# Performance work log

Hardware: AMD Instinct MI355X
Metric: run time of the kernel (lower is better)

## Reference

```python
import jax, jax.numpy as jnp
import numpy as np

B, T, N, F, O = 4, 8192, 64, 16, 32  # batch, timesteps, vertices, in_feat, out_feat


def setup_inputs() -> dict:
    key = jax.random.key(0)
    ks = jax.random.split(key, 8)
    return {
        "x": jax.random.normal(ks[0], (B, T, N * F), dtype=jnp.float32),
        "adj": jax.random.uniform(ks[1], (N, N), dtype=jnp.float32),
        "W1": jax.random.normal(ks[2], (T,), dtype=jnp.float32) / np.sqrt(T).astype(np.float32),
        "W2": jax.random.normal(ks[3], (F, T), dtype=jnp.float32) / np.sqrt(F).astype(np.float32),
        "W3": jax.random.normal(ks[4], (F,), dtype=jnp.float32) / np.sqrt(F).astype(np.float32),
        "bs": jax.random.normal(ks[5], (1, N, N), dtype=jnp.float32) * 0.02,
        "Vs": jax.random.normal(ks[6], (N, N), dtype=jnp.float32) * 0.02,
        "conv_w": jax.random.normal(ks[7], (O, N * F, 3), dtype=jnp.float32) * 0.02,
    }


def reference(x, adj, W1, W2, W3, bs, Vs, conv_w):
    bz, t, _ = x.shape
    x4 = x.reshape(bz, t, N, F)
    xp = jnp.transpose(x4, (0, 2, 3, 1))  # (B, N, F, T)

    # Spatial attention: S in (B, N, N)
    lhs = jnp.einsum('bnft,t->bnf', xp, W1) @ W2          # (B, N, T)
    rhs = jnp.einsum('f,bnft->bnt', W3, xp)               # (B, N, T)
    product = jnp.einsum('bnt,bmt->bnm', lhs, rhs)        # (B, N, N)
    S = jnp.einsum('nm,bmk->bnk', Vs, jax.nn.sigmoid(product + bs))
    S = jax.nn.softmax(S, axis=1)

    # Apply attention over the vertex dim
    xr = jnp.transpose(x4, (0, 1, 3, 2)).reshape(bz, t * F, N)  # (B, T*F, N)
    xm = jnp.einsum('bpn,bnm->bpm', xr, S)                      # (B, T*F, N)
    xf = jnp.transpose(xm.reshape(bz, t, F, N), (0, 2, 1, 3))   # (B, F, T, N)

    # einsum 'bftn,nn->bftn' == scale by diagonal of adj
    xf = xf * jnp.diagonal(adj)                                 # broadcast over N

    xo = jnp.transpose(xf, (0, 2, 3, 1)).reshape(bz, t, N * F)  # (B, T, N*F)

    # Conv1d(kernel=3, padding=1, no bias), channels-last
    out = jax.lax.conv_general_dilated(
        xo, conv_w,
        window_strides=(1,), padding=((1, 1),),
        dimension_numbers=('NWC', 'OIW', 'NWC'))
    return out  # (B, T, O)
```

## Files before the change

### kernel.cpp

```cpp
#include <hip/hip_runtime.h>
#include <hip/hip_bf16.h>

#define B_ 4
#define T_ 8192
#define N_ 64
#define F_ 16
#define O_ 32

typedef _Float16 half8_t __attribute__((ext_vector_type(8)));
typedef _Float16 half4_t __attribute__((ext_vector_type(4)));
typedef float float4_t __attribute__((ext_vector_type(4)));

#define WS_A1G  0
#define WS_SSC  32768
#define WS_WFT  98304
#define WS_P    524288
#define WS_XH   9437184
#define XH_BYTES ((size_t)B_ * (T_ + 2) * 1024 * sizeof(_Float16))

#define TB_ 32

__global__ __launch_bounds__(256) void kA2(const float* __restrict__ x,
                                           const float* __restrict__ W1,
                                           const float* __restrict__ W2,
                                           const float* __restrict__ W3,
                                           float* __restrict__ P,
                                           _Float16* __restrict__ xh) {
    __shared__ float w2s[16][TB_ + 1];
    __shared__ float w1s[TB_];
    const int b    = blockIdx.x >> 8;
    const int tile = blockIdx.x & 255;
    const int t0   = tile * TB_;
    const int tid  = threadIdx.x;
    const int fq   = tid & 3;

    for (int i = tid; i < 16 * TB_; i += 256) {
        const int f = i >> 5, r = i & 31;
        w2s[f][r] = W2[f * T_ + t0 + r];
    }
    if (tid < TB_) w1s[tid] = W1[t0 + tid];
    __syncthreads();

    float w3v[4];
#pragma unroll
    for (int j = 0; j < 4; ++j) w3v[j] = W3[fq * 4 + j];

    const float* xbase = x + ((size_t)b * T_ + t0) * 1024 + tid * 4;
    _Float16* xrow = xh ? (xh + ((size_t)b * (T_ + 2) + (t0 + 1)) * 1024 + tid * 4)
                        : (_Float16*)nullptr;
    float4_t accA = {0.f, 0.f, 0.f, 0.f};
    float4_t accG = {0.f, 0.f, 0.f, 0.f};

#pragma unroll 8
    for (int r = 0; r < TB_; ++r) {
        float4_t xv = *(const float4_t*)(xbase + (size_t)r * 1024);
        if (xh) {
            half4_t hv;
            hv[0] = (_Float16)xv[0]; hv[1] = (_Float16)xv[1];
            hv[2] = (_Float16)xv[2]; hv[3] = (_Float16)xv[3];
            *(half4_t*)(xrow + (size_t)r * 1024) = hv;
        }
        float v = xv[0] * w3v[0] + xv[1] * w3v[1] + xv[2] * w3v[2] + xv[3] * w3v[3];
        v += __shfl_xor(v, 1);
        v += __shfl_xor(v, 2);
        const float w1r = w1s[r];
#pragma unroll
        for (int j = 0; j < 4; ++j) {
            accA[j] += w1r * xv[j];
            accG[j] += w2s[fq * 4 + j][r] * v;
        }
    }

    if (xh) {
        half4_t z = {(_Float16)0.f, (_Float16)0.f, (_Float16)0.f, (_Float16)0.f};
        if (tile == 0)
            *(half4_t*)(xh + (size_t)b * (T_ + 2) * 1024 + tid * 4) = z;
        if (tile == 255)
            *(half4_t*)(xh + ((size_t)b * (T_ + 2) + T_ + 1) * 1024 + tid * 4) = z;
    }

    float* pb = P + (size_t)blockIdx.x * 2048 + tid * 4;
    *(float4_t*)pb          = accA;
    *(float4_t*)(pb + 1024) = accG;
}

__global__ __launch_bounds__(256) void kR(const float* __restrict__ P,
                                          float* __restrict__ A1G) {
    const int b   = blockIdx.x >> 3;
    const int seg = blockIdx.x & 7;
    const int tid = threadIdx.x;
    const int o4  = tid & 63;
    const int g   = tid >> 6;

    const float* base = P + (size_t)b * 256 * 2048 + seg * 256 + o4 * 4;
    float4_t s = {0.f, 0.f, 0.f, 0.f};
#pragma unroll 4
    for (int tt = 0; tt < 64; ++tt) {
        float4_t v = *(const float4_t*)(base + (size_t)(g * 64 + tt) * 2048);
        s += v;
    }

    __shared__ float4_t red[4][64];
    red[g][o4] = s;
    __syncthreads();
    if (tid < 64) {
        float4_t t = red[0][tid] + red[1][tid] + red[2][tid] + red[3][tid];
        *(float4_t*)(A1G + (size_t)b * 2048 + seg * 256 + tid * 4) = t;
    }
}

__global__ __launch_bounds__(256) void kC(const float* __restrict__ A1G,
                                          const float* __restrict__ bs,
                                          const float* __restrict__ Vs,
                                          const float* __restrict__ adj,
                                          float* __restrict__ Ssc) {
    const int b = blockIdx.x;
    __shared__ float a1[64][17], g[64][17];
    __shared__ float sig[64][64];
    __shared__ float vs[64][64];
    __shared__ float redmx[4][64];
    __shared__ float redsm[4][64];
    const int tid = threadIdx.x;

    for (int i = tid; i < 1024; i += 256) {
        a1[i >> 4][i & 15] = A1G[b * 2048 + i];
        g [i >> 4][i & 15] = A1G[b * 2048 + 1024 + i];
    }
    for (int i = tid; i < 4096; i += 256) vs[i >> 6][i & 63] = Vs[i];
    __syncthreads();

#pragma unroll
    for (int i = 0; i < 16; ++i) {
        const int e = tid + 256 * i, r = e >> 6, c = e & 63;
        float p = 0.f;
#pragma unroll
        for (int f = 0; f < 16; ++f) p += a1[r][f] * g[c][f];
        p += bs[e];
        sig[r][c] = 1.f / (1.f + __expf(-p));
    }
    __syncthreads();

    const int gw = tid >> 6;
    const int c  = tid & 63;
    const int r0 = gw * 16;

    float sc_[64];
#pragma unroll
    for (int m = 0; m < 64; ++m) sc_[m] = sig[m][c];

    float acc[16];
#pragma unroll
    for (int rl = 0; rl < 16; ++rl) {
        const float4_t* vr = (const float4_t*)&vs[r0 + rl][0];
        float sA = 0.f, sB = 0.f, sC = 0.f, sD = 0.f;
#pragma unroll
        for (int m4 = 0; m4 < 4; ++m4) {
            float4_t v0 = vr[m4];
            float4_t v1 = vr[m4 + 4];
            float4_t v2 = vr[m4 + 8];
            float4_t v3 = vr[m4 + 12];
#pragma unroll
            for (int j = 0; j < 4; ++j) {
                sA += v0[j] * sc_[m4 * 4 + j];
                sB += v1[j] * sc_[16 + m4 * 4 + j];
                sC += v2[j] * sc_[32 + m4 * 4 + j];
                sD += v3[j] * sc_[48 + m4 * 4 + j];
            }
        }
        acc[rl] = (sA + sB) + (sC + sD);
    }

    float pmax = -1e30f;
#pragma unroll
    for (int rl = 0; rl < 16; ++rl) pmax = fmaxf(pmax, acc[rl]);
    redmx[gw][c] = pmax;
    __syncthreads();
    const float mx = fmaxf(fmaxf(redmx[0][c], redmx[1][c]),
                           fmaxf(redmx[2][c], redmx[3][c]));

    float psum = 0.f;
#pragma unroll
    for (int rl = 0; rl < 16; ++rl) {
        acc[rl] = __expf(acc[rl] - mx);
        psum += acc[rl];
    }
    redsm[gw][c] = psum;
    __syncthreads();
    const float sum = (redsm[0][c] + redsm[1][c]) + (redsm[2][c] + redsm[3][c]);
    const float scl = adj[c * 64 + c] / sum;

#pragma unroll
    for (int rl = 0; rl < 16; ++rl)
        Ssc[b * 4096 + (r0 + rl) * 64 + c] = acc[rl] * scl;
}

__global__ __launch_bounds__(256) void kD(const float* __restrict__ Ssc,
                                          const float* __restrict__ conv_w,
                                          _Float16* __restrict__ Wft) {
    const int b = blockIdx.x >> 5, o = blockIdx.x & 31;
    __shared__ float ssc[4096];
    __shared__ float cw[3072];
    const int tid = threadIdx.x;
    for (int i = tid; i < 4096; i += 256) ssc[i] = Ssc[b * 4096 + i];
    for (int i = tid; i < 3072; i += 256) cw[i] = conv_w[o * 3072 + i];
    __syncthreads();

#pragma unroll
    for (int i = 0; i < 12; ++i) {
        const int e = tid + 256 * i;
        const int k = e >> 10, rem = e & 1023, m = rem >> 4, f = rem & 15;
        float s = 0.f;
#pragma unroll
        for (int n = 0; n < 64; ++n) s += cw[(n * 16 + f) * 3 + k] * ssc[m * 64 + n];
        Wft[(size_t)(b * 32 + o) * 3072 + e] = (_Float16)s;
    }
}

__global__ __launch_bounds__(256) void kE16(const _Float16* __restrict__ xh,
                                            const _Float16* __restrict__ Wft,
                                            float* __restrict__ out) {
    const int b    = blockIdx.x >> 7;
    const int tile = blockIdx.x & 127;
    const int wave = threadIdx.x >> 6;
    const int lane = threadIdx.x & 63;
    const int q = lane >> 4, l = lane & 15;
    const int t0 = tile * 64 + wave * 16;

    const _Float16* wb0 = Wft + (size_t)(b * 32 + l) * 3072;
    const _Float16* wb1 = wb0 + 16 * 3072;
    const _Float16* xb = xh + ((size_t)b * (T_ + 2) + (t0 + l)) * 1024 + q * 8;

    float4_t acc0 = {0.f, 0.f, 0.f, 0.f};
    float4_t acc1 = {0.f, 0.f, 0.f, 0.f};

#pragma unroll 8
    for (int kk = 0; kk < 96; ++kk) {
        const int K  = kk * 32;
        const int kc = K >> 10;
        const int c0 = K & 1023;

        half8_t af  = *(const half8_t*)(xb + (size_t)kc * 1024 + c0);
        half8_t bf0 = *(const half8_t*)(wb0 + K + q * 8);
        half8_t bf1 = *(const half8_t*)(wb1 + K + q * 8);

        acc0 = __builtin_amdgcn_mfma_f32_16x16x32_f16(af, bf0, acc0, 0, 0, 0);
        acc1 = __builtin_amdgcn_mfma_f32_16x16x32_f16(af, bf1, acc1, 0, 0, 0);
    }

#pragma unroll
    for (int rg = 0; rg < 4; ++rg) {
        const int t = t0 + q * 4 + rg;
        float* op = out + ((size_t)b * T_ + t) * 32;
        op[l]      = acc0[rg];
        op[16 + l] = acc1[rg];
    }
}

__global__ __launch_bounds__(256) void kE32(const float* __restrict__ x,
                                            const _Float16* __restrict__ Wft,
                                            float* __restrict__ out) {
    const int b    = blockIdx.x >> 7;
    const int tile = blockIdx.x & 127;
    const int wave = threadIdx.x >> 6;
    const int lane = threadIdx.x & 63;
    const int q = lane >> 4, l = lane & 15;
    const int t0 = tile * 64 + wave * 16;

    const _Float16* wb0 = Wft + (size_t)(b * 32 + l) * 3072;
    const _Float16* wb1 = wb0 + 16 * 3072;
    const float* xb = x + (size_t)b * T_ * 1024;

    float4_t acc0 = {0.f, 0.f, 0.f, 0.f};
    float4_t acc1 = {0.f, 0.f, 0.f, 0.f};

#pragma unroll 4
    for (int kk = 0; kk < 96; ++kk) {
        const int K  = kk * 32;
        const int kc = K >> 10;
        const int c0 = (K & 1023) + q * 8;
        const int row = t0 + l + kc - 1;
        const bool valid = (unsigned)row < (unsigned)T_;
        const int rc = valid ? row : 0;
        const float sc = valid ? 1.f : 0.f;

        const float* ap = xb + (size_t)rc * 1024 + c0;
        float4_t a0 = *(const float4_t*)ap;
        float4_t a1 = *(const float4_t*)(ap + 4);

        half8_t af;
        af[0] = (_Float16)(a0[0] * sc); af[1] = (_Float16)(a0[1] * sc);
        af[2] = (_Float16)(a0[2] * sc); af[3] = (_Float16)(a0[3] * sc);
        af[4] = (_Float16)(a1[0] * sc); af[5] = (_Float16)(a1[1] * sc);
        af[6] = (_Float16)(a1[2] * sc); af[7] = (_Float16)(a1[3] * sc);

        half8_t bf0 = *(const half8_t*)(wb0 + K + q * 8);
        half8_t bf1 = *(const half8_t*)(wb1 + K + q * 8);

        acc0 = __builtin_amdgcn_mfma_f32_16x16x32_f16(af, bf0, acc0, 0, 0, 0);
        acc1 = __builtin_amdgcn_mfma_f32_16x16x32_f16(af, bf1, acc1, 0, 0, 0);
    }

#pragma unroll
    for (int rg = 0; rg < 4; ++rg) {
        const int t = t0 + q * 4 + rg;
        float* op = out + ((size_t)b * T_ + t) * 32;
        op[l]      = acc0[rg];
        op[16 + l] = acc1[rg];
    }
}

extern "C" void kernel_launch(void* const* d_in, const int* in_sizes, int n_in,
                              void* d_out, int out_size, void* d_ws, size_t ws_size,
                              hipStream_t stream) {
    const float* x      = (const float*)d_in[0];
    const float* adj    = (const float*)d_in[1];
    const float* W1     = (const float*)d_in[2];
    const float* W2     = (const float*)d_in[3];
    const float* W3     = (const float*)d_in[4];
    const float* bs     = (const float*)d_in[5];
    const float* Vs     = (const float*)d_in[6];
    const float* conv_w = (const float*)d_in[7];
    float* out = (float*)d_out;

    char* ws = (char*)d_ws;
    float*    A1G = (float*)(ws + WS_A1G);
    float*    Ssc = (float*)(ws + WS_SSC);
    _Float16* Wft = (_Float16*)(ws + WS_WFT);
    float*    P   = (float*)(ws + WS_P);

    const bool use16 = ws_size >= (size_t)WS_XH + XH_BYTES;
    _Float16* xh = use16 ? (_Float16*)(ws + WS_XH) : (_Float16*)nullptr;

    kA2<<<B_ * (T_ / TB_), 256, 0, stream>>>(x, W1, W2, W3, P, xh);
    kR <<<B_ * 8,          256, 0, stream>>>(P, A1G);
    kC <<<B_,              256, 0, stream>>>(A1G, bs, Vs, adj, Ssc);
    kD <<<B_ * O_,         256, 0, stream>>>(Ssc, conv_w, Wft);
    if (use16) kE16<<<B_ * (T_ / 64), 256, 0, stream>>>(xh, Wft, out);
    else       kE32<<<B_ * (T_ / 64), 256, 0, stream>>>(x, Wft, out);
}
```

Before: 319.1 us.

## Halve time tiles, remap kA2 threads per vertex, split kE16 waves by output half

kA2 now handles 16 timesteps per block instead of 32, which doubles its grid. Each thread processes a full 16-feature vertex row across 4 timesteps, so the shuffle reduction is gone, and partial sums are combined across waves in shared memory before being written out. kR is adjusted for the doubled partial count. kE16 gives each wave one 16-output half for 16 timesteps, which doubles its grid and halves per-wave work. The change aims to raise parallelism and occupancy in the bandwidth-bound passes. In exchange, A-fragment loads in kE16 are duplicated across the two output halves, kA2 uses more registers, and P grows, which needs a larger workspace.

```diff
diff --git a/kernel.cpp b/kernel.cpp
--- a/kernel.cpp
+++ b/kernel.cpp
@@ -15,84 +15,127 @@
 #define WS_SSC  32768
 #define WS_WFT  98304
 #define WS_P    524288
-#define WS_XH   9437184
+#define WS_XH   17825792
 #define XH_BYTES ((size_t)B_ * (T_ + 2) * 1024 * sizeof(_Float16))
 
-#define TB_ 32
-
-__global__ __launch_bounds__(256) void kA2(const float* __restrict__ x,
-                                           const float* __restrict__ W1,
-                                           const float* __restrict__ W2,
-                                           const float* __restrict__ W3,
-                                           float* __restrict__ P,
-                                           _Float16* __restrict__ xh) {
+#define TB_ 16
+
+__global__ __launch_bounds__(256, 6) void kA2(const float* __restrict__ x,
+                                              const float* __restrict__ W1,
+                                              const float* __restrict__ W2,
+                                              const float* __restrict__ W3,
+                                              float* __restrict__ P,
+                                              _Float16* __restrict__ xh) {
     __shared__ float w2s[16][TB_ + 1];
     __shared__ float w1s[TB_];
-    const int b    = blockIdx.x >> 8;
-    const int tile = blockIdx.x & 255;
+    __shared__ float red[4][64][16];
+    const int b    = blockIdx.x >> 9;
+    const int tile = blockIdx.x & 511;
     const int t0   = tile * TB_;
     const int tid  = threadIdx.x;
-    const int fq   = tid & 3;
-
-    for (int i = tid; i < 16 * TB_; i += 256) {
-        const int f = i >> 5, r = i & 31;
+    const int w    = tid >> 6;
+    const int n    = tid & 63;
+
+    {
+        const int f = tid >> 4, r = tid & 15;
         w2s[f][r] = W2[f * T_ + t0 + r];
-    }
-    if (tid < TB_) w1s[tid] = W1[t0 + tid];
-    __syncthreads();
-
-    float w3v[4];
-#pragma unroll
-    for (int j = 0; j < 4; ++j) w3v[j] = W3[fq * 4 + j];
-
-    const float* xbase = x + ((size_t)b * T_ + t0) * 1024 + tid * 4;
-    _Float16* xrow = xh ? (xh + ((size_t)b * (T_ + 2) + (t0 + 1)) * 1024 + tid * 4)
-                        : (_Float16*)nullptr;
-    float4_t accA = {0.f, 0.f, 0.f, 0.f};
-    float4_t accG = {0.f, 0.f, 0.f, 0.f};
-
-#pragma unroll 8
-    for (int r = 0; r < TB_; ++r) {
-        float4_t xv = *(const float4_t*)(xbase + (size_t)r * 1024);
+        if (tid < TB_) w1s[tid] = W1[t0 + tid];
+    }
+    __syncthreads();
+
+    float w3v[16];
+#pragma unroll
+    for (int f = 0; f < 16; ++f) w3v[f] = W3[f];
+
+    float accA[16], accG[16];
+#pragma unroll
+    for (int f = 0; f < 16; ++f) { accA[f] = 0.f; accG[f] = 0.f; }
+
+    const float* xrow0 = x + ((size_t)b * T_ + t0 + w * 4) * 1024 + n * 16;
+    _Float16* xh0 = xh ? (xh + ((size_t)b * (T_ + 2) + t0 + 1 + w * 4) * 1024 + n * 16)
+                       : (_Float16*)nullptr;
+
+#pragma unroll
+    for (int i = 0; i < 4; ++i) {
+        const int r = w * 4 + i;
+        const float* xp = xrow0 + (size_t)i * 1024;
+        float4_t x0 = *(const float4_t*)(xp);
+        float4_t x1 = *(const float4_t*)(xp + 4);
+        float4_t x2 = *(const float4_t*)(xp + 8);
+        float4_t x3 = *(const float4_t*)(xp + 12);
+
         if (xh) {
-            half4_t hv;
-            hv[0] = (_Float16)xv[0]; hv[1] = (_Float16)xv[1];
-            hv[2] = (_Float16)xv[2]; hv[3] = (_Float16)xv[3];
-            *(half4_t*)(xrow + (size_t)r * 1024) = hv;
+            half8_t h0, h1;
+#pragma unroll
+            for (int j = 0; j < 4; ++j) {
+                h0[j]     = (_Float16)x0[j]; h0[4 + j] = (_Float16)x1[j];
+                h1[j]     = (_Float16)x2[j]; h1[4 + j] = (_Float16)x3[j];
+            }
+            _Float16* hp = xh0 + (size_t)i * 1024;
+            *(half8_t*)(hp)     = h0;
+            *(half8_t*)(hp + 8) = h1;
         }
-        float v = xv[0] * w3v[0] + xv[1] * w3v[1] + xv[2] * w3v[2] + xv[3] * w3v[3];
-        v += __shfl_xor(v, 1);
-        v += __shfl_xor(v, 2);
+
+        float v = 0.f;
+#pragma unroll
+        for (int j = 0; j < 4; ++j) {
+            v += x0[j] * w3v[j]      + x1[j] * w3v[4 + j]
+               + x2[j] * w3v[8 + j]  + x3[j] * w3v[12 + j];
+        }
         const float w1r = w1s[r];
 #pragma unroll
         for (int j = 0; j < 4; ++j) {
-            accA[j] += w1r * xv[j];
-            accG[j] += w2s[fq * 4 + j][r] * v;
+            accA[j]      += w1r * x0[j];  accA[4 + j]  += w1r * x1[j];
+            accA[8 + j]  += w1r * x2[j];  accA[12 + j] += w1r * x3[j];
         }
+#pragma unroll
+        for (int f = 0; f < 16; ++f) accG[f] += w2s[f][r] * v;
     }
 
     if (xh) {
         half4_t z = {(_Float16)0.f, (_Float16)0.f, (_Float16)0.f, (_Float16)0.f};
         if (tile == 0)
             *(half4_t*)(xh + (size_t)b * (T_ + 2) * 1024 + tid * 4) = z;
-        if (tile == 255)
+        if (tile == 511)
             *(half4_t*)(xh + ((size_t)b * (T_ + 2) + T_ + 1) * 1024 + tid * 4) = z;
     }
 
-    float* pb = P + (size_t)blockIdx.x * 2048 + tid * 4;
-    *(float4_t*)pb          = accA;
-    *(float4_t*)(pb + 1024) = accG;
+#pragma unroll
+    for (int f = 0; f < 16; ++f) red[w][n][f] = accA[f];
+    __syncthreads();
+    {
+        const int nn = tid >> 2, fb = (tid & 3) * 4;
+        float4_t s;
+#pragma unroll
+        for (int j = 0; j < 4; ++j)
+            s[j] = red[0][nn][fb + j] + red[1][nn][fb + j]
+                 + red[2][nn][fb + j] + red[3][nn][fb + j];
+        *(float4_t*)(P + (size_t)blockIdx.x * 2048 + nn * 16 + fb) = s;
+    }
+    __syncthreads();
+#pragma unroll
+    for (int f = 0; f < 16; ++f) red[w][n][f] = accG[f];
+    __syncthreads();
+    {
+        const int nn = tid >> 2, fb = (tid & 3) * 4;
+        float4_t s;
+#pragma unroll
+        for (int j = 0; j < 4; ++j)
+            s[j] = red[0][nn][fb + j] + red[1][nn][fb + j]
+                 + red[2][nn][fb + j] + red[3][nn][fb + j];
+        *(float4_t*)(P + (size_t)blockIdx.x * 2048 + 1024 + nn * 16 + fb) = s;
+    }
 }
 
 __global__ __launch_bounds__(256) void kR(const float* __restrict__ P,
                                           float* __restrict__ A1G) {
-    const int b   = blockIdx.x >> 3;
-    const int seg = blockIdx.x & 7;
+    const int b   = blockIdx.x >> 4;
+    const int seg = blockIdx.x & 15;
     const int tid = threadIdx.x;
-    const int o4  = tid & 63;
-    const int g   = tid >> 6;
-
-    const float* base = P + (size_t)b * 256 * 2048 + seg * 256 + o4 * 4;
+    const int o4  = tid & 31;
+    const int g   = tid >> 5;
+
+    const float* base = P + (size_t)b * 512 * 2048 + seg * 128 + o4 * 4;
     float4_t s = {0.f, 0.f, 0.f, 0.f};
 #pragma unroll 4
     for (int tt = 0; tt < 64; ++tt) {
@@ -100,12 +143,14 @@
         s += v;
     }
 
-    __shared__ float4_t red[4][64];
+    __shared__ float4_t red[8][32];
     red[g][o4] = s;
     __syncthreads();
-    if (tid < 64) {
-        float4_t t = red[0][tid] + red[1][tid] + red[2][tid] + red[3][tid];
-        *(float4_t*)(A1G + (size_t)b * 2048 + seg * 256 + tid * 4) = t;
+    if (tid < 32) {
+        float4_t t = {0.f, 0.f, 0.f, 0.f};
+#pragma unroll
+        for (int gg = 0; gg < 8; ++gg) t += red[gg][tid];
+        *(float4_t*)(A1G + (size_t)b * 2048 + seg * 128 + tid * 4) = t;
     }
 }
 
@@ -219,19 +264,18 @@
 __global__ __launch_bounds__(256) void kE16(const _Float16* __restrict__ xh,
                                             const _Float16* __restrict__ Wft,
                                             float* __restrict__ out) {
-    const int b    = blockIdx.x >> 7;
-    const int tile = blockIdx.x & 127;
+    const int b    = blockIdx.x >> 8;
+    const int tile = blockIdx.x & 255;
     const int wave = threadIdx.x >> 6;
     const int lane = threadIdx.x & 63;
     const int q = lane >> 4, l = lane & 15;
-    const int t0 = tile * 64 + wave * 16;
-
-    const _Float16* wb0 = Wft + (size_t)(b * 32 + l) * 3072;
-    const _Float16* wb1 = wb0 + 16 * 3072;
+    const int tq = wave >> 1, oh = wave & 1;
+    const int t0 = tile * 32 + tq * 16;
+
+    const _Float16* wb = Wft + (size_t)(b * 32 + oh * 16 + l) * 3072;
     const _Float16* xb = xh + ((size_t)b * (T_ + 2) + (t0 + l)) * 1024 + q * 8;
 
-    float4_t acc0 = {0.f, 0.f, 0.f, 0.f};
-    float4_t acc1 = {0.f, 0.f, 0.f, 0.f};
+    float4_t acc = {0.f, 0.f, 0.f, 0.f};
 
 #pragma unroll 8
     for (int kk = 0; kk < 96; ++kk) {
@@ -239,20 +283,15 @@
         const int kc = K >> 10;
         const int c0 = K & 1023;
 
-        half8_t af  = *(const half8_t*)(xb + (size_t)kc * 1024 + c0);
-        half8_t bf0 = *(const half8_t*)(wb0 + K + q * 8);
-        half8_t bf1 = *(const half8_t*)(wb1 + K + q * 8);
-
-        acc0 = __builtin_amdgcn_mfma_f32_16x16x32_f16(af, bf0, acc0, 0, 0, 0);
-        acc1 = __builtin_amdgcn_mfma_f32_16x16x32_f16(af, bf1, acc1, 0, 0, 0);
+        half8_t af = *(const half8_t*)(xb + (size_t)kc * 1024 + c0);
+        half8_t bf = *(const half8_t*)(wb + K + q * 8);
+        acc = __builtin_amdgcn_mfma_f32_16x16x32_f16(af, bf, acc, 0, 0, 0);
     }
 
 #pragma unroll
     for (int rg = 0; rg < 4; ++rg) {
         const int t = t0 + q * 4 + rg;
-        float* op = out + ((size_t)b * T_ + t) * 32;
-        op[l]      = acc0[rg];
-        op[16 + l] = acc1[rg];
+        out[((size_t)b * T_ + t) * 32 + oh * 16 + l] = acc[rg];
     }
 }
 
@@ -332,9 +371,9 @@
     _Float16* xh = use16 ? (_Float16*)(ws + WS_XH) : (_Float16*)nullptr;
 
     kA2<<<B_ * (T_ / TB_), 256, 0, stream>>>(x, W1, W2, W3, P, xh);
-    kR <<<B_ * 8,          256, 0, stream>>>(P, A1G);
+    kR <<<B_ * 16,         256, 0, stream>>>(P, A1G);
     kC <<<B_,              256, 0, stream>>>(A1G, bs, Vs, adj, Ssc);
     kD <<<B_ * O_,         256, 0, stream>>>(Ssc, conv_w, Wft);
-    if (use16) kE16<<<B_ * (T_ / 64), 256, 0, stream>>>(xh, Wft, out);
+    if (use16) kE16<<<B_ * (T_ / 32), 256, 0, stream>>>(xh, Wft, out);
     else       kE32<<<B_ * (T_ / 64), 256, 0, stream>>>(x, Wft, out);
 }
```

After: 391.7 us. 1.23x slower.

## Halve tile sizes in reduction and GEMM kernels to raise block counts

Applied to the files above, without the earlier changes.

The first-pass reduction kernel now processes 16 timesteps per block instead of 32, doubling its grid, and the partial-sum workspace and the reduction kernel are resized to match. The final MFMA kernel now gives each wave one 16-wide output half instead of both halves, with each block covering 32 timesteps, again doubling the grid. The aim is more blocks and waves in flight to fill the GPU's compute units, at the cost of reading the fp16 activations twice per timestep tile and a larger partial-sum buffer to reduce.

```diff
diff --git a/kernel.cpp b/kernel.cpp
--- a/kernel.cpp
+++ b/kernel.cpp
@@ -15,10 +15,10 @@
 #define WS_SSC  32768
 #define WS_WFT  98304
 #define WS_P    524288
-#define WS_XH   9437184
+#define WS_XH   17825792
 #define XH_BYTES ((size_t)B_ * (T_ + 2) * 1024 * sizeof(_Float16))
 
-#define TB_ 32
+#define TB_ 16
 
 __global__ __launch_bounds__(256) void kA2(const float* __restrict__ x,
                                            const float* __restrict__ W1,
@@ -28,17 +28,17 @@
                                            _Float16* __restrict__ xh) {
     __shared__ float w2s[16][TB_ + 1];
     __shared__ float w1s[TB_];
-    const int b    = blockIdx.x >> 8;
-    const int tile = blockIdx.x & 255;
+    const int b    = blockIdx.x >> 9;
+    const int tile = blockIdx.x & 511;
     const int t0   = tile * TB_;
     const int tid  = threadIdx.x;
     const int fq   = tid & 3;
 
-    for (int i = tid; i < 16 * TB_; i += 256) {
-        const int f = i >> 5, r = i & 31;
+    {
+        const int f = tid >> 4, r = tid & 15;
         w2s[f][r] = W2[f * T_ + t0 + r];
-    }
-    if (tid < TB_) w1s[tid] = W1[t0 + tid];
+        if (tid < TB_) w1s[tid] = W1[t0 + tid];
+    }
     __syncthreads();
 
     float w3v[4];
@@ -46,19 +46,19 @@
     for (int j = 0; j < 4; ++j) w3v[j] = W3[fq * 4 + j];
 
     const float* xbase = x + ((size_t)b * T_ + t0) * 1024 + tid * 4;
-    _Float16* xrow = xh ? (xh + ((size_t)b * (T_ + 2) + (t0 + 1)) * 1024 + tid * 4)
-                        : (_Float16*)nullptr;
+    _Float16* xhb = xh ? (xh + ((size_t)b * (T_ + 2) + t0 + 1) * 1024 + tid * 4)
+                       : (_Float16*)nullptr;
     float4_t accA = {0.f, 0.f, 0.f, 0.f};
     float4_t accG = {0.f, 0.f, 0.f, 0.f};
 
-#pragma unroll 8
+#pragma unroll
     for (int r = 0; r < TB_; ++r) {
         float4_t xv = *(const float4_t*)(xbase + (size_t)r * 1024);
         if (xh) {
             half4_t hv;
             hv[0] = (_Float16)xv[0]; hv[1] = (_Float16)xv[1];
             hv[2] = (_Float16)xv[2]; hv[3] = (_Float16)xv[3];
-            *(half4_t*)(xrow + (size_t)r * 1024) = hv;
+            *(half4_t*)(xhb + (size_t)r * 1024) = hv;
         }
         float v = xv[0] * w3v[0] + xv[1] * w3v[1] + xv[2] * w3v[2] + xv[3] * w3v[3];
         v += __shfl_xor(v, 1);
@@ -75,7 +75,7 @@
         half4_t z = {(_Float16)0.f, (_Float16)0.f, (_Float16)0.f, (_Float16)0.f};
         if (tile == 0)
             *(half4_t*)(xh + (size_t)b * (T_ + 2) * 1024 + tid * 4) = z;
-        if (tile == 255)
+        if (tile == 511)
             *(half4_t*)(xh + ((size_t)b * (T_ + 2) + T_ + 1) * 1024 + tid * 4) = z;
     }
 
@@ -86,26 +86,28 @@
 
 __global__ __launch_bounds__(256) void kR(const float* __restrict__ P,
                                           float* __restrict__ A1G) {
-    const int b   = blockIdx.x >> 3;
-    const int seg = blockIdx.x & 7;
+    const int b   = blockIdx.x >> 5;
+    const int seg = blockIdx.x & 31;
     const int tid = threadIdx.x;
-    const int o4  = tid & 63;
-    const int g   = tid >> 6;
-
-    const float* base = P + (size_t)b * 256 * 2048 + seg * 256 + o4 * 4;
+    const int o4  = tid & 15;
+    const int g   = tid >> 4;
+
+    const float* base = P + (size_t)b * 512 * 2048 + seg * 64 + o4 * 4;
     float4_t s = {0.f, 0.f, 0.f, 0.f};
 #pragma unroll 4
-    for (int tt = 0; tt < 64; ++tt) {
-        float4_t v = *(const float4_t*)(base + (size_t)(g * 64 + tt) * 2048);
+    for (int tt = 0; tt < 32; ++tt) {
+        float4_t v = *(const float4_t*)(base + (size_t)(g * 32 + tt) * 2048);
         s += v;
     }
 
-    __shared__ float4_t red[4][64];
+    __shared__ float4_t red[16][16];
     red[g][o4] = s;
     __syncthreads();
-    if (tid < 64) {
-        float4_t t = red[0][tid] + red[1][tid] + red[2][tid] + red[3][tid];
-        *(float4_t*)(A1G + (size_t)b * 2048 + seg * 256 + tid * 4) = t;
+    if (tid < 16) {
+        float4_t t = {0.f, 0.f, 0.f, 0.f};
+#pragma unroll
+        for (int gg = 0; gg < 16; ++gg) t += red[gg][tid];
+        *(float4_t*)(A1G + (size_t)b * 2048 + seg * 64 + tid * 4) = t;
     }
 }
 
@@ -219,19 +221,18 @@
 __global__ __launch_bounds__(256) void kE16(const _Float16* __restrict__ xh,
                                             const _Float16* __restrict__ Wft,
                                             float* __restrict__ out) {
-    const int b    = blockIdx.x >> 7;
-    const int tile = blockIdx.x & 127;
+    const int b    = blockIdx.x >> 8;
+    const int tile = blockIdx.x & 255;
     const int wave = threadIdx.x >> 6;
     const int lane = threadIdx.x & 63;
     const int q = lane >> 4, l = lane & 15;
-    const int t0 = tile * 64 + wave * 16;
-
-    const _Float16* wb0 = Wft + (size_t)(b * 32 + l) * 3072;
-    const _Float16* wb1 = wb0 + 16 * 3072;
+    const int tq = wave >> 1, oh = wave & 1;
+    const int t0 = tile * 32 + tq * 16;
+
+    const _Float16* wb = Wft + (size_t)(b * 32 + oh * 16 + l) * 3072;
     const _Float16* xb = xh + ((size_t)b * (T_ + 2) + (t0 + l)) * 1024 + q * 8;
 
-    float4_t acc0 = {0.f, 0.f, 0.f, 0.f};
-    float4_t acc1 = {0.f, 0.f, 0.f, 0.f};
+    float4_t acc = {0.f, 0.f, 0.f, 0.f};
 
 #pragma unroll 8
     for (int kk = 0; kk < 96; ++kk) {
@@ -239,20 +240,15 @@
         const int kc = K >> 10;
         const int c0 = K & 1023;
 
-        half8_t af  = *(const half8_t*)(xb + (size_t)kc * 1024 + c0);
-        half8_t bf0 = *(const half8_t*)(wb0 + K + q * 8);
-        half8_t bf1 = *(const half8_t*)(wb1 + K + q * 8);
-
-        acc0 = __builtin_amdgcn_mfma_f32_16x16x32_f16(af, bf0, acc0, 0, 0, 0);
-        acc1 = __builtin_amdgcn_mfma_f32_16x16x32_f16(af, bf1, acc1, 0, 0, 0);
+        half8_t af = *(const half8_t*)(xb + (size_t)kc * 1024 + c0);
+        half8_t bf = *(const half8_t*)(wb + K + q * 8);
+        acc = __builtin_amdgcn_mfma_f32_16x16x32_f16(af, bf, acc, 0, 0, 0);
     }
 
 #pragma unroll
     for (int rg = 0; rg < 4; ++rg) {
         const int t = t0 + q * 4 + rg;
-        float* op = out + ((size_t)b * T_ + t) * 32;
-        op[l]      = acc0[rg];
-        op[16 + l] = acc1[rg];
+        out[((size_t)b * T_ + t) * 32 + oh * 16 + l] = acc[rg];
     }
 }
 
@@ -332,9 +328,9 @@
     _Float16* xh = use16 ? (_Float16*)(ws + WS_XH) : (_Float16*)nullptr;
 
     kA2<<<B_ * (T_ / TB_), 256, 0, stream>>>(x, W1, W2, W3, P, xh);
-    kR <<<B_ * 8,          256, 0, stream>>>(P, A1G);
+    kR <<<B_ * 32,         256, 0, stream>>>(P, A1G);
     kC <<<B_,              256, 0, stream>>>(A1G, bs, Vs, adj, Ssc);
     kD <<<B_ * O_,         256, 0, stream>>>(Ssc, conv_w, Wft);
-    if (use16) kE16<<<B_ * (T_ / 64), 256, 0, stream>>>(xh, Wft, out);
+    if (use16) kE16<<<B_ * (T_ / 32), 256, 0, stream>>>(xh, Wft, out);
     else       kE32<<<B_ * (T_ / 64), 256, 0, stream>>>(x, Wft, out);
 }
```

Measured after the change: 364.5 us. 14.2% more time.
